# Kernel tuning notes

Hardware: AMD Instinct MI355X
Metric: run time of the kernel (lower is better)

The kernel has to match this reference:

```python
import jax, jax.numpy as jnp
import numpy as np
from jax import lax

B, T_Y, T_X = 16, 1600, 400
MEL_C, TXT_C, MAS_C = 80, 512, 384
HID = MAS_C * 2          # SwiGLUConvFFN hidden width (mas_channels*2)
NEG = -1e9


def setup_inputs() -> dict:
    key = jax.random.key(0)
    ks = jax.random.split(key, 20)
    p = lambda k, s: jax.random.normal(k, s, jnp.float32) * 0.02
    return {
        "mel_hidden_states": jax.random.normal(ks[0], (B, T_Y, MEL_C), jnp.float32),
        "text_hidden_states": jax.random.normal(ks[1], (B, T_X, TXT_C), jnp.float32),
        # mel SwiGLU conv-FFN (kernel 5): in->2*HID, gate, HID->MAS_C
        "mel_w1": p(ks[2], (2 * HID, MEL_C, 5)), "mel_b1": jnp.zeros((2 * HID,), jnp.float32),
        "mel_w2": p(ks[3], (MAS_C, HID, 5)),     "mel_b2": jnp.zeros((MAS_C,), jnp.float32),
        # text SwiGLU conv-FFN (kernel 3)
        "txt_w1": p(ks[4], (2 * HID, TXT_C, 3)), "txt_b1": jnp.zeros((2 * HID,), jnp.float32),
        "txt_w2": p(ks[5], (MAS_C, HID, 3)),     "txt_b2": jnp.zeros((MAS_C,), jnp.float32),
        # SimpleAttention query/key projections (value proj does not affect returned outputs)
        "wq": p(ks[6], (MAS_C, MAS_C)), "bq": jnp.zeros((MAS_C,), jnp.float32),
        "wk": p(ks[7], (MAS_C, MAS_C)), "bk": jnp.zeros((MAS_C,), jnp.float32),
        "x_lens": jax.random.randint(ks[8], (B,), T_X // 2, T_X + 1).astype(jnp.int32),
        "y_lens": jax.random.randint(ks[9], (B,), T_Y // 2, T_Y + 1).astype(jnp.int32),
    }


def _conv_ffn(x, pad_mask, w1, b1, w2, b2):
    """SwiGLU/ReGLU conv FFN. x:(B,T,C), pad_mask:(B,T) True=padded."""
    keep = (~pad_mask)[:, None, :].astype(x.dtype)          # (B,1,T)
    h = jnp.transpose(x, (0, 2, 1)) * keep                  # (B,C,T)
    dn = ("NCH", "OIH", "NCH")
    h = lax.conv_general_dilated(h, w1, (1,), "SAME", dimension_numbers=dn) + b1[None, :, None]
    a, g = jnp.split(h, 2, axis=1)
    h = a * jax.nn.relu(g) * keep                           # relugt gating
    h = lax.conv_general_dilated(h, w2, (1,), "SAME", dimension_numbers=dn) + b2[None, :, None]
    return jnp.transpose(h * keep, (0, 2, 1))               # (B,T,out)


def _mas_single(logp, t_x, t_y):
    """Glow-TTS maximum_path for one item. logp:(T_X,T_Y). Returns hard path (T_X,T_Y)."""
    xi = jnp.arange(T_X)
    yi = jnp.arange(T_Y)
    valid = (xi[:, None] < t_x) & (yi[None, :] < t_y) & (xi[:, None] <= yi[None, :])
    lp = jnp.where(valid, logp, NEG)

    def fstep(prev, col):                                   # prev:(T_X,), col:(T_X,)
        shifted = jnp.concatenate([jnp.full((1,), NEG, prev.dtype), prev[:-1]])
        cur = col + jnp.maximum(prev, shifted)
        return cur, cur

    init = jnp.where(xi == 0, 0.0, NEG).astype(logp.dtype)
    _, v = lax.scan(fstep, init, lp.T)                      # v:(T_Y,T_X) DP table

    def bstep(x, y):                                        # backtrack from y=T_Y-1 down
        active = y < t_y
        row = (xi == x) & active
        vp = v[y - 1]
        dec = (x > 0) & ((x == y) | (vp[jnp.maximum(x - 1, 0)] > vp[x]))
        new_x = jnp.where(active & (y > 0) & dec, x - 1, x)
        return new_x, row

    _, rows = lax.scan(bstep, t_x - 1, jnp.arange(T_Y - 1, -1, -1))
    return rows[::-1].T.astype(jnp.float32)                 # (T_X,T_Y)


def _safe_log(t, eps=1e-6):
    return jnp.nan_to_num(jnp.log(t + eps), nan=eps)


def reference(mel_hidden_states, text_hidden_states,
              mel_w1, mel_b1, mel_w2, mel_b2,
              txt_w1, txt_b1, txt_w2, txt_b2,
              wq, bq, wk, bk, x_lens, y_lens):
    x_mask = jnp.arange(T_X)[None, :] >= x_lens[:, None]    # (B,T_X) True=padded
    y_mask = jnp.arange(T_Y)[None, :] >= y_lens[:, None]    # (B,T_Y)

    text_proj = _conv_ffn(text_hidden_states, x_mask, txt_w1, txt_b1, txt_w2, txt_b2)
    mel_proj = _conv_ffn(mel_hidden_states, y_mask, mel_w1, mel_b1, mel_w2, mel_b2)

    q = mel_proj @ wq.T + bq                                # (B,T_Y,D)
    k = text_proj @ wk.T + bk                               # (B,T_X,D)
    scores = jnp.einsum("byd,bxd->byx", q, k) / (MAS_C ** 0.5)
    # expand_masks: mask==0 only where query AND key are both padded (faithful to source)
    both_pad = y_mask[:, :, None] & x_mask[:, None, :]
    scores = jnp.where(both_pad, jnp.float32(-1e-9), scores)
    attn_w = jax.nn.softmax(scores, axis=-1)                # (B,T_Y,T_X)

    avg_attn = attn_w[:, None]                              # (B,1,T_Y,T_X)
    attn_logprob = _safe_log(avg_attn)

    mas_in = jnp.transpose(attn_logprob[:, 0], (0, 2, 1))   # (B,T_X,T_Y)
    attn_hard = lax.stop_gradient(jax.vmap(_mas_single)(mas_in, x_lens, y_lens))
    attn_hard_dur = attn_hard.sum(2)                        # (B,T_X)
    return avg_attn, attn_logprob, attn_hard, attn_hard_dur
```

## Files before the change

### kernel.cpp

```cpp
#include <hip/hip_runtime.h>
#include <cstdint>

#define B 16
#define TY 1600
#define TX 400
#define MAS 384
#define HID 768
#define NEGV -1e9f

typedef __bf16 bf16x8 __attribute__((ext_vector_type(8)));
typedef float  f32x4  __attribute__((ext_vector_type(4)));
typedef float  f32x16 __attribute__((ext_vector_type(16)));

__device__ __forceinline__ f32x4 mfma16(bf16x8 a, bf16x8 b, f32x4 c) {
  return __builtin_amdgcn_mfma_f32_16x16x32_bf16(a, b, c, 0, 0, 0);
}
__device__ __forceinline__ f32x16 mfma32(bf16x8 a, bf16x8 b, f32x16 c) {
  return __builtin_amdgcn_mfma_f32_32x32x16_bf16(a, b, c, 0, 0, 0);
}

__global__ void split_pad_k(const float* __restrict__ in, __bf16* __restrict__ oh,
                            __bf16* __restrict__ ol, int CIN, int CINP, long n) {
  long i = (long)blockIdx.x * 256 + threadIdx.x;
  if (i >= n) return;
  long row = i / CINP; int ci = (int)(i - row * CINP);
  float v = (ci < CIN) ? in[row * CIN + ci] : 0.f;
  __bf16 h = (__bf16)v;
  oh[i] = h; ol[i] = (__bf16)(v - (float)h);
}

__global__ void wsplit_k(const float* __restrict__ w, __bf16* __restrict__ oh,
                         __bf16* __restrict__ ol, int CIN, int K_, int CINP, long n) {
  long i = (long)blockIdx.x * 256 + threadIdx.x;
  if (i >= n) return;
  long kdspan = (long)K_ * CINP;
  long nn = i / kdspan; int kd = (int)(i - nn * kdspan);
  int k = kd / CINP, ci = kd - k * CINP;
  float v = (ci < CIN) ? w[(nn * CIN + ci) * K_ + k] : 0.f;
  __bf16 h = (__bf16)v;
  oh[i] = h; ol[i] = (__bf16)(v - (float)h);
}

__global__ void tsplit_k(const float* __restrict__ in, __bf16* __restrict__ oh,
                         __bf16* __restrict__ ol, int JTOT, long n) {
  long i = (long)blockIdx.x * 256 + threadIdx.x;
  if (i >= n) return;
  int m = (int)(i / JTOT), j = (int)(i - (long)m * JTOT);
  float v = in[i];
  long o = (long)j * 384 + m;
  __bf16 h = (__bf16)v;
  oh[o] = h; ol[o] = (__bf16)(v - (float)h);
}

__global__ void fold_bias_k(const float* __restrict__ wq, const float* __restrict__ b,
                            float* __restrict__ o) {
  int n = threadIdx.x;
  float s = 0.f;
  for (int m = 0; m < 384; ++m) s = fmaf(wq[n * 384 + m], b[m], s);
  o[n] = s;
}

template<int KK>
__global__ __launch_bounds__(256)
void fold_mfma(const __bf16* __restrict__ xh, const __bf16* __restrict__ xl,
               const __bf16* __restrict__ wh, const __bf16* __restrict__ wl,
               __bf16* __restrict__ oh, __bf16* __restrict__ ol)
{
  constexpr int CINP = 384, ROWS = 64, STRIDE = 65;
  __shared__ float4 xs[8 * STRIDE];
  const int t0 = blockIdx.x * 64, n0 = blockIdx.y * 128;
  const int tid = threadIdx.x, wn = tid >> 6, lane = tid & 63;
  const int lr = lane & 15, lg = lane >> 4;
  const f32x4 Z4 = {0.f, 0.f, 0.f, 0.f};
  f32x4 acc[4][2];
  #pragma unroll
  for (int m = 0; m < 4; ++m) { acc[m][0] = Z4; acc[m][1] = Z4; }

  #pragma unroll 1
  for (int ci0 = 0; ci0 < CINP; ci0 += 32) {
    __syncthreads();
    for (int e = tid; e < ROWS * 8; e += 256) {
      int row = e >> 3, sc = e & 7, spl = sc >> 2, cg = sc & 3;
      int t = t0 + row;
      xs[(spl * 4 + cg) * STRIDE + row] =
          *(const float4*)((spl ? xl : xh) + (size_t)t * CINP + ci0 + cg * 8);
    }
    __syncthreads();
    bf16x8 ah[4], al[4];
    #pragma unroll
    for (int mf = 0; mf < 4; ++mf) {
      int row = mf * 16 + lr;
      ah[mf] = *(const bf16x8*)&xs[lg * STRIDE + row];
      al[mf] = *(const bf16x8*)&xs[(4 + lg) * STRIDE + row];
    }
    size_t kd = (size_t)ci0 + lg * 8;
    bf16x8 bh[2], bl[2];
    #pragma unroll
    for (int nf = 0; nf < 2; ++nf) {
      int nc = n0 + wn * 32 + nf * 16 + lr;
      bh[nf] = *(const bf16x8*)(wh + (size_t)nc * 384 + kd);
      bl[nf] = *(const bf16x8*)(wl + (size_t)nc * 384 + kd);
    }
    #pragma unroll
    for (int nf = 0; nf < 2; ++nf)
      #pragma unroll
      for (int mf = 0; mf < 4; ++mf) acc[mf][nf] = mfma16(ah[mf], bh[nf], acc[mf][nf]);
    #pragma unroll
    for (int nf = 0; nf < 2; ++nf)
      #pragma unroll
      for (int mf = 0; mf < 4; ++mf) acc[mf][nf] = mfma16(ah[mf], bl[nf], acc[mf][nf]);
    #pragma unroll
    for (int nf = 0; nf < 2; ++nf)
      #pragma unroll
      for (int mf = 0; mf < 4; ++mf) acc[mf][nf] = mfma16(al[mf], bh[nf], acc[mf][nf]);
  }
  #pragma unroll
  for (int nf = 0; nf < 2; ++nf) {
    int c = n0 + wn * 32 + nf * 16 + lr;
    #pragma unroll
    for (int mf = 0; mf < 4; ++mf) {
      #pragma unroll
      for (int r = 0; r < 4; ++r) {
        int j = t0 + mf * 16 + lg * 4 + r;
        int k = j % KK, ci = j / KK;
        size_t o = (size_t)((((ci >> 4) * KK + k) * 2 + ((ci >> 3) & 1)) * 3072)
                 + (size_t)c * 8 + (ci & 7);
        float v = acc[mf][nf][r];
        __bf16 vh = (__bf16)v;
        oh[o] = vh; ol[o] = (__bf16)(v - (float)vh);
      }
    }
  }
}

template<int CINP, int K, int T>
__global__ __launch_bounds__(256)
void conv1_mfma(const __bf16* __restrict__ xh, const __bf16* __restrict__ xl,
                const __bf16* __restrict__ wh, const __bf16* __restrict__ wl,
                const float* __restrict__ bias, const int* __restrict__ lens,
                __bf16* __restrict__ hh, __bf16* __restrict__ hl)
{
  constexpr int BM = 128, PAD = K / 2, ROWS = BM + K - 1, KD = K * CINP;
  __shared__ float4 xs[8 * ROWS];
  const int b = blockIdx.z, t0 = blockIdx.x * BM, n0 = blockIdx.y * 64;
  const int tid = threadIdx.x, wid = tid >> 6, lane = tid & 63;
  const int wm = wid >> 1, wn = wid & 1, lr = lane & 15, lg = lane >> 4;
  const int len = lens[b];
  const f32x4 Z4 = {0.f, 0.f, 0.f, 0.f};
  f32x4 acc_a[4][2], acc_g[4][2];
  #pragma unroll
  for (int m = 0; m < 4; ++m)
    #pragma unroll
    for (int n = 0; n < 2; ++n) { acc_a[m][n] = Z4; acc_g[m][n] = Z4; }

  #pragma unroll 1
  for (int ci0 = 0; ci0 < CINP; ci0 += 32) {
    __syncthreads();
    for (int e = tid; e < ROWS * 8; e += 256) {
      int row = e >> 3, sc = e & 7, spl = sc >> 2, cg = sc & 3;
      int t = t0 + row - PAD;
      float4 v = {0.f, 0.f, 0.f, 0.f};
      if (t >= 0 && t < len)
        v = *(const float4*)((spl ? xl : xh) + ((size_t)b * T + t) * CINP + ci0 + cg * 8);
      xs[(spl * 4 + cg) * ROWS + row] = v;
    }
    __syncthreads();
    #pragma unroll
    for (int k = 0; k < K; ++k) {
      bf16x8 ah[4], al[4];
      #pragma unroll
      for (int mf = 0; mf < 4; ++mf) {
        int row = wm * 64 + mf * 16 + lr + k;
        ah[mf] = *(const bf16x8*)&xs[lg * ROWS + row];
        al[mf] = *(const bf16x8*)&xs[(4 + lg) * ROWS + row];
      }
      size_t kd = (size_t)k * CINP + ci0 + lg * 8;
      #pragma unroll
      for (int nf = 0; nf < 2; ++nf) {
        int na = n0 + wn * 32 + nf * 16 + lr;
        bf16x8 bah = *(const bf16x8*)(wh + (size_t)na * KD + kd);
        bf16x8 bal = *(const bf16x8*)(wl + (size_t)na * KD + kd);
        bf16x8 bgh = *(const bf16x8*)(wh + (size_t)(na + HID) * KD + kd);
        bf16x8 bgl = *(const bf16x8*)(wl + (size_t)(na + HID) * KD + kd);
        #pragma unroll
        for (int mf = 0; mf < 4; ++mf) {
          acc_a[mf][nf] = mfma16(ah[mf], bah, acc_a[mf][nf]);
          acc_a[mf][nf] = mfma16(ah[mf], bal, acc_a[mf][nf]);
          acc_a[mf][nf] = mfma16(al[mf], bah, acc_a[mf][nf]);
          acc_g[mf][nf] = mfma16(ah[mf], bgh, acc_g[mf][nf]);
          acc_g[mf][nf] = mfma16(ah[mf], bgl, acc_g[mf][nf]);
          acc_g[mf][nf] = mfma16(al[mf], bgh, acc_g[mf][nf]);
        }
      }
    }
  }
  #pragma unroll
  for (int nf = 0; nf < 2; ++nf) {
    int c = n0 + wn * 32 + nf * 16 + lr;
    float ba = bias[c], bg = bias[c + HID];
    #pragma unroll
    for (int mf = 0; mf < 4; ++mf) {
      #pragma unroll
      for (int r = 0; r < 4; ++r) {
        int t = t0 + wm * 64 + mf * 16 + lg * 4 + r;
        if (t < T) {
          float a = acc_a[mf][nf][r] + ba;
          float g = acc_g[mf][nf][r] + bg;
          float v = a * fmaxf(g, 0.f);
          __bf16 vh = (__bf16)v;
          size_t o = ((size_t)b * T + t) * HID + c;
          hh[o] = vh;
          hl[o] = (__bf16)(v - (float)vh);
        }
      }
    }
  }
}

template<int K, int T, bool STORET>
__global__ __launch_bounds__(256)
void conv2_mfma(const __bf16* __restrict__ xh, const __bf16* __restrict__ xl,
                const __bf16* __restrict__ wh, const __bf16* __restrict__ wl,
                const float* __restrict__ bias, const float* __restrict__ ab,
                const int* __restrict__ lens, float* __restrict__ out)
{
  constexpr int CINP = 768, BM = 128, PAD = K / 2, ROWS = BM + K - 1, STRIDE = ROWS + 1;
  constexpr int BROWS = K * 2;
  __shared__ float4 xa[4 * STRIDE];
  __shared__ float4 bs[2 * BROWS * 192];
  const int b = blockIdx.z, t0 = blockIdx.x * BM, n0 = blockIdx.y * 192;
  const int tid = threadIdx.x, wid = tid >> 6, lane = tid & 63;
  const int wm = wid >> 1, wn = wid & 1, lc = lane & 31, lk = lane >> 5;
  const int len = lens[b];
  f32x16 acc[2][3];
  #pragma unroll
  for (int m = 0; m < 2; ++m)
    #pragma unroll
    for (int n = 0; n < 3; ++n)
      #pragma unroll
      for (int r = 0; r < 16; ++r) acc[m][n][r] = 0.f;

  #pragma unroll 1
  for (int s = 0; s < 48; ++s) {
    __syncthreads();
    for (int e = tid; e < ROWS * 4; e += 256) {
      int row = e >> 2, sc = e & 3, spl = sc >> 1, cg = sc & 1;
      int t = t0 + row - PAD;
      float4 v = {0.f, 0.f, 0.f, 0.f};
      if (t >= 0 && t < len)
        v = *(const float4*)((spl ? xl : xh) + ((size_t)b * T + t) * CINP + s * 16 + cg * 8);
      xa[(spl * 2 + cg) * STRIDE + row] = v;
    }
    for (int r = wid; r < 2 * BROWS; r += 4) {
      int spl = r / BROWS, rr = r - spl * BROWS;
      const char* src = (const char*)((spl ? wl : wh) + (size_t)(s * BROWS + rr) * 3072
                                      + (size_t)n0 * 8) + (size_t)lane * 16;
      char* dst = (char*)&bs[r * 192];
      #pragma unroll
      for (int i = 0; i < 3; ++i)
        __builtin_amdgcn_global_load_lds(
            (const __attribute__((address_space(1))) void*)(src + i * 1024),
            (__attribute__((address_space(3))) void*)(dst + i * 1024), 16, 0, 0);
    }
    __syncthreads();
    #pragma unroll
    for (int k = 0; k < K; ++k) {
      bf16x8 ah[2], al[2], bh[3], bl[3];
      #pragma unroll
      for (int mf = 0; mf < 2; ++mf) {
        int row = wm * 64 + mf * 32 + lc + k;
        ah[mf] = *(const bf16x8*)&xa[lk * STRIDE + row];
        al[mf] = *(const bf16x8*)&xa[(2 + lk) * STRIDE + row];
      }
      #pragma unroll
      for (int nf = 0; nf < 3; ++nf) {
        int col = wn * 96 + nf * 32 + lc;
        bh[nf] = *(const bf16x8*)&bs[(k * 2 + lk) * 192 + col];
        bl[nf] = *(const bf16x8*)&bs[(BROWS + k * 2 + lk) * 192 + col];
      }
      #pragma unroll
      for (int nf = 0; nf < 3; ++nf)
        #pragma unroll
        for (int mf = 0; mf < 2; ++mf)
          acc[mf][nf] = mfma32(ah[mf], bh[nf], acc[mf][nf]);
      #pragma unroll
      for (int nf = 0; nf < 3; ++nf)
        #pragma unroll
        for (int mf = 0; mf < 2; ++mf)
          acc[mf][nf] = mfma32(ah[mf], bl[nf], acc[mf][nf]);
      #pragma unroll
      for (int nf = 0; nf < 3; ++nf)
        #pragma unroll
        for (int mf = 0; mf < 2; ++mf)
          acc[mf][nf] = mfma32(al[mf], bh[nf], acc[mf][nf]);
    }
  }
  #pragma unroll
  for (int nf = 0; nf < 3; ++nf) {
    int c = n0 + wn * 96 + nf * 32 + lc;
    float bb = bias[c], aB = ab[c];
    #pragma unroll
    for (int mf = 0; mf < 2; ++mf) {
      #pragma unroll
      for (int r = 0; r < 16; ++r) {
        int t = t0 + wm * 64 + mf * 32 + (r & 3) + 8 * (r >> 2) + 4 * lk;
        if (t < T) {
          float v = acc[mf][nf][r] + bb;
          if (t >= len) v = 0.f;
          v += aB;
          if (STORET) out[((size_t)b * MAS + c) * T + t] = v;
          else        out[((size_t)b * T + t) * MAS + c] = v;
        }
      }
    }
  }
}

__global__ __launch_bounds__(512)
void scores_k(const float* __restrict__ q, const float* __restrict__ kT,
              const int* __restrict__ xl, const int* __restrict__ yl,
              float* __restrict__ oattn, float* __restrict__ ologp)
{
  __shared__ float qs[16 * 384];
  __shared__ float tmp[8];
  const int b = blockIdx.y, y0 = blockIdx.x * 16, tid = threadIdx.x;
  for (int e = tid; e < 16 * 384; e += 512)
    qs[e] = q[((size_t)b * TY + (y0 + e / 384)) * 384 + (e - (e / 384) * 384)];
  __syncthreads();
  float acc[16];
  #pragma unroll
  for (int i = 0; i < 16; ++i) acc[i] = 0.f;
  const int x = tid;
  if (x < TX) {
    const float* kb = kT + (size_t)b * MAS * TX + x;
    for (int d = 0; d < 384; d += 4) {
      float k0 = kb[(size_t)(d + 0) * TX], k1 = kb[(size_t)(d + 1) * TX];
      float k2 = kb[(size_t)(d + 2) * TX], k3 = kb[(size_t)(d + 3) * TX];
      #pragma unroll
      for (int yy = 0; yy < 16; ++yy) {
        float4 qv = *(const float4*)&qs[yy * 384 + d];
        acc[yy] = fmaf(qv.x, k0, fmaf(qv.y, k1, fmaf(qv.z, k2, fmaf(qv.w, k3, acc[yy]))));
      }
    }
  }
  const int xlen = xl[b], ylen = yl[b];
  const float scale = 0.05103103630798288f;
  const bool xpad = (x >= xlen);
  const int wv = tid >> 6, ln = tid & 63;
  #pragma unroll 1
  for (int yy = 0; yy < 16; ++yy) {
    int y = y0 + yy;
    float s = -3.0e38f;
    if (x < TX) {
      s = acc[yy] * scale;
      if (xpad && (y >= ylen)) s = -1e-9f;
    }
    float m = s;
    for (int off = 32; off; off >>= 1) m = fmaxf(m, __shfl_xor(m, off));
    if (ln == 0) tmp[wv] = m;
    __syncthreads();
    float mx = fmaxf(fmaxf(fmaxf(tmp[0], tmp[1]), fmaxf(tmp[2], tmp[3])),
                     fmaxf(fmaxf(tmp[4], tmp[5]), fmaxf(tmp[6], tmp[7])));
    __syncthreads();
    float e = (x < TX) ? expf(s - mx) : 0.f;
    float sm = e;
    for (int off = 32; off; off >>= 1) sm += __shfl_xor(sm, off);
    if (ln == 0) tmp[wv] = sm;
    __syncthreads();
    float tot = tmp[0] + tmp[1] + tmp[2] + tmp[3] + tmp[4] + tmp[5] + tmp[6] + tmp[7];
    __syncthreads();
    if (x < TX) {
      float w = e / tot;
      size_t o = ((size_t)b * TY + y) * TX + x;
      oattn[o] = w;
      ologp[o] = logf(w + 1e-6f);
    }
  }
}

#define MLD4(sbv, Lbuf) do {                                              \
    _Pragma("unroll")                                                     \
    for (int r_ = 0; r_ < 4; ++r_) {                                      \
      const int row_ = (sbv) * 4 + r_;                                    \
      Lbuf[r_][0] = *(const float2*)&half[row_ * 400 + a0];               \
      Lbuf[r_][1] = *(const float2*)&half[row_ * 400 + a1];               \
      Lbuf[r_][2] = *(const float2*)&half[row_ * 400 + a2];               \
    } } while (0)

#define MCMP4(sbv, Lbuf) do {                                             \
    _Pragma("unroll")                                                     \
    for (int r_ = 0; r_ < 4; ++r_) {                                      \
      const int y_ = ybase + (sbv) * 4 + r_;                              \
      float lp[6] = {Lbuf[r_][0].x + wxm[0], Lbuf[r_][0].y + wxm[1],      \
                     Lbuf[r_][1].x + wxm[2], Lbuf[r_][1].y + wxm[3],      \
                     Lbuf[r_][2].x + wxm[4], Lbuf[r_][2].y + wxm[5]};     \
      if (phase1) {                                                       \
        int c_ = y_ - p0;                                                 \
        _Pragma("unroll")                                                 \
        for (int j_ = 0; j_ < 6; ++j_) lp[j_] = (j_ <= c_) ? lp[j_] : NEGV; \
      }                                                                   \
      unsigned pr_ = ((w[3] > w[4]) ? 1u : 0u) | ((w[4] > w[5]) ? 2u : 0u); \
      p16 |= pr_ << ((y_ & 7) * 2);                                       \
      float nw[6];                                                        \
      nw[0] = lp[0] + w[0];                                               \
      _Pragma("unroll")                                                   \
      for (int j_ = 1; j_ < 6; ++j_) nw[j_] = lp[j_] + fmaxf(w[j_], w[j_ - 1]); \
      _Pragma("unroll")                                                   \
      for (int j_ = 0; j_ < 6; ++j_) w[j_] = nw[j_];                      \
    } } while (0)

#define FLUSHBITS(y7_) do {                                               \
    unsigned lo = 0, hi = 0;                                              \
    _Pragma("unroll")                                                     \
    for (int r2_ = 0; r2_ < 4; ++r2_) {                                   \
      lo |= ((p16 >> (2 * r2_)) & 3u) << (8 * r2_);                       \
      hi |= ((p16 >> (2 * r2_ + 8)) & 3u) << (8 * r2_);                   \
    }                                                                     \
    unsigned lo1 = (unsigned)__shfl_xor((int)lo, 1), hi1 = (unsigned)__shfl_xor((int)hi, 1); \
    lo |= lo1 << 2; hi |= hi1 << 2;                                       \
    unsigned lo2 = (unsigned)__shfl_xor((int)lo, 2), hi2 = (unsigned)__shfl_xor((int)hi, 2); \
    lo |= lo2 << 4; hi |= hi2 << 4;                                       \
    if ((GL & 3) == 0 && GL < 200) {                                      \
      unsigned long long E = (unsigned long long)lo | ((unsigned long long)hi << 32); \
      *(unsigned long long*)&lbits[(size_t)((y7_) >> 3) * 512 + (size_t)(GL >> 2) * 8] = E; \
    }                                                                     \
    p16 = 0; } while (0)

#define LBAR() do {                                                       \
    asm volatile("s_waitcnt lgkmcnt(0)" ::: "memory");                    \
    __builtin_amdgcn_sched_barrier(0);                                    \
    __builtin_amdgcn_s_barrier();                                         \
    __builtin_amdgcn_sched_barrier(0); } while (0)

#define PUBEX() do {                                                      \
    if (GL < 200) { vbuf[pb][2 * GL] = w[4]; vbuf[pb][2 * GL + 1] = w[5]; } \
    LBAR();                                                               \
    _Pragma("unroll")                                                     \
    for (int j_ = 0; j_ < 4; ++j_) {                                      \
      int x_ = p0 + j_;                                                   \
      w[j_] = (x_ >= 0 && GL < 200) ? vbuf[pb][x_] : NEGV;                \
    }                                                                     \
    pb ^= 1; } while (0)

__global__ __launch_bounds__(256, 1)
void mas_k(const float* __restrict__ logprob, const int* __restrict__ xl,
           const int* __restrict__ yl, float* __restrict__ hard, float* __restrict__ dur)
{
  __shared__ float ring[12800];
  __shared__ unsigned char lbits[102400];
  __shared__ float vbuf[2][400];
  const int b = blockIdx.x;
  const int tid = threadIdx.x, wid = tid >> 6;
  const int GL = tid;
  const int xlen = xl[b], ylen = yl[b];
  const float* lpb = logprob + (size_t)b * TY * TX;
  const int p0 = GL * 2 - 4;

  int a0 = p0, a1 = p0 + 2, a2 = p0 + 4;
  a0 = a0 < 0 ? 0 : (a0 > 398 ? 398 : a0);
  a1 = a1 < 0 ? 0 : (a1 > 398 ? 398 : a1);
  a2 = a2 < 0 ? 0 : (a2 > 398 ? 398 : a2);

  float w[6], wxm[6];
  #pragma unroll
  for (int j = 0; j < 6; ++j) {
    int x = p0 + j;
    wxm[j] = (x >= 0 && x < xlen) ? 0.f : NEGV;
    w[j] = (x == 0) ? 0.f : NEGV;
  }

  const char* lpc = (const char*)lpb;
  constexpr size_t maxgs = (size_t)TY * 1600 - 25600;
  char* ringc = (char*)ring;
  const int lane = tid & 63;
  auto issue_group = [&](int g) {
    size_t gs = (size_t)g * 25600; if (gs > maxgs) gs = maxgs;
    for (int c = wid; c < 25; c += 4)
      __builtin_amdgcn_global_load_lds(
          (const __attribute__((address_space(1))) void*)(lpc + gs + (size_t)c * 1024 + (size_t)lane * 16),
          (__attribute__((address_space(3))) void*)(ringc + (g & 1) * 25600 + c * 1024), 16, 0, 0);
  };

  issue_group(0);
  issue_group(1);

  int pb = 0;
  unsigned p16 = 0;
  const int ngroups = (ylen + 15) >> 4;
  #pragma unroll 1
  for (int g = 0; g < ngroups; ++g) {
    if (wid == 0) asm volatile("s_waitcnt vmcnt(7)" ::: "memory");
    else          asm volatile("s_waitcnt vmcnt(6)" ::: "memory");
    __builtin_amdgcn_sched_barrier(0);
    __builtin_amdgcn_s_barrier();
    __builtin_amdgcn_sched_barrier(0);
    const float* half = ring + (g & 1) * 6400;
    const int ybase = g * 16;
    const bool phase1 = (ybase < TX);
    float2 LA[4][3], LB[4][3];
    MLD4(0, LA);
    MCMP4(0, LA);
    MLD4(1, LB);
    PUBEX();
    MCMP4(1, LB);
    FLUSHBITS(ybase + 7);
    MLD4(2, LA);
    PUBEX();
    MCMP4(2, LA);
    MLD4(3, LB);
    PUBEX();
    MCMP4(3, LB);
    FLUSHBITS(ybase + 15);
    PUBEX();
    __builtin_amdgcn_sched_barrier(0);
    issue_group(g + 2);
  }

  __syncthreads();
  if (wid != 0) return;

  int x = xlen - 1;
  int cnt = 0;
  float* hb = hard + (size_t)b * TX * TY;
  float* db = dur + (size_t)b * TX;

  #pragma unroll 1
  for (int ycur = ylen - 1; ycur >= 0; ycur -= 64) {
    int lo = x - 63; if (lo < 0) lo = 0;
    const int wb = (lo >> 3) & ~3;
    int ry = ycur - lane;
    unsigned w0 = 0, w1 = 0, w2 = 0;
    if (ry >= 0) {
      const unsigned char* p = lbits + (size_t)(ry >> 3) * 512 + (ry & 7);
      unsigned bt_[12];
      #pragma unroll
      for (int j = 0; j < 12; ++j) bt_[j] = p[(size_t)(wb + j) * 8];
      w0 = bt_[0] | (bt_[1] << 8) | (bt_[2] << 16) | (bt_[3] << 24);
      w1 = bt_[4] | (bt_[5] << 8) | (bt_[6] << 16) | (bt_[7] << 24);
      w2 = bt_[8] | (bt_[9] << 8) | (bt_[10] << 16) | (bt_[11] << 24);
    }
    const int rows = (ycur + 1 < 64) ? (ycur + 1) : 64;
    #pragma unroll 1
    for (int s = 0; s < rows; s += 8) {
      const int cnt8 = (rows - s < 8) ? (rows - s) : 8;
      unsigned r0[8], r1[8], r2[8];
      #pragma unroll
      for (int u = 0; u < 8; ++u) {
        r0[u] = (unsigned)__builtin_amdgcn_readlane((int)w0, s + u);
        r1[u] = (unsigned)__builtin_amdgcn_readlane((int)w1, s + u);
        r2[u] = (unsigned)__builtin_amdgcn_readlane((int)w2, s + u);
      }
      #pragma unroll
      for (int u = 0; u < 8; ++u) {
        if (u < cnt8) {
          const int yy = ycur - s - u;
          ++cnt;
          if (yy > 0 && x > 0) {
            const int boff = (x >> 3) - wb;
            const unsigned word = (boff < 4) ? r0[u] : ((boff < 8) ? r1[u] : r2[u]);
            const unsigned byte = word >> ((boff & 3) * 8);
            if ((x == yy) || ((byte >> (x & 7)) & 1)) {
              for (int q = lane; q < cnt; q += 64) hb[(size_t)x * TY + yy + q] = 1.0f;
              if (lane == 0) db[x] = (float)cnt;
              cnt = 0;
              --x;
            }
          }
        }
      }
    }
  }
  for (int q = lane; q < cnt; q += 64) hb[(size_t)x * TY + q] = 1.0f;
  if (lane == 0) db[x] = (float)cnt;
}

extern "C" void kernel_launch(void* const* d_in, const int* in_sizes, int n_in,
                              void* d_out, int out_size, void* d_ws, size_t ws_size,
                              hipStream_t stream) {
  const float* mel_x  = (const float*)d_in[0];
  const float* txt_x  = (const float*)d_in[1];
  const float* mel_w1 = (const float*)d_in[2];
  const float* mel_b1 = (const float*)d_in[3];
  const float* mel_w2 = (const float*)d_in[4];
  const float* mel_b2 = (const float*)d_in[5];
  const float* txt_w1 = (const float*)d_in[6];
  const float* txt_b1 = (const float*)d_in[7];
  const float* txt_w2 = (const float*)d_in[8];
  const float* txt_b2 = (const float*)d_in[9];
  const float* wq     = (const float*)d_in[10];
  const float* bq     = (const float*)d_in[11];
  const float* wk     = (const float*)d_in[12];
  const float* bk     = (const float*)d_in[13];
  const int*   xl     = (const int*)d_in[14];
  const int*   yl     = (const int*)d_in[15];

  char* wsb = (char*)d_ws;
  constexpr size_t MXH   = 0;
  constexpr size_t MXL   = MXH   + 4915200;
  constexpr size_t TXH   = MXL   + 4915200;
  constexpr size_t TXL   = TXH   + 6553600;
  constexpr size_t KTF   = TXH;
  constexpr size_t WFMH  = TXL   + 6553600;
  constexpr size_t WFML  = WFMH  + 2949120;
  constexpr size_t WFTH  = WFML  + 2949120;
  constexpr size_t WFTL  = WFTH  + 1769472;
  constexpr size_t B2M   = WFTL  + 1769472;
  constexpr size_t B2T   = B2M   + 2048;
  constexpr size_t HH    = B2T   + 2048;
  constexpr size_t HL    = HH    + 39321600;
  constexpr size_t SCR   = HL    + 39321600;
  constexpr size_t W1MH  = SCR;
  constexpr size_t W1ML  = W1MH  + 1474560;
  constexpr size_t W1TH  = W1ML  + 1474560;
  constexpr size_t W1TL  = W1TH  + 4718592;
  constexpr size_t WQH   = W1TL  + 4718592;
  constexpr size_t WQL   = WQH   + 294912;
  constexpr size_t WKH   = WQL   + 294912;
  constexpr size_t WKL   = WKH   + 294912;
  constexpr size_t W2TMH = WKL   + 294912;
  constexpr size_t W2TML = W2TMH + 2949120;
  constexpr size_t W2TTH = W2TML + 2949120;
  constexpr size_t W2TTL = W2TTH + 1769472;
  constexpr size_t QF    = SCR;

  float* out = (float*)d_out;
  float* o_attn = out;
  float* o_logp = out + (size_t)10240000;
  float* o_hard = out + (size_t)20480000;
  float* o_dur  = out + (size_t)30720000;

  hipMemsetAsync(o_hard, 0, (size_t)(10240000 + 6400) * sizeof(float), stream);

  split_pad_k<<<9600, 256, 0, stream>>>(mel_x, (__bf16*)(wsb + MXH), (__bf16*)(wsb + MXL), 80, 96, 2457600L);
  split_pad_k<<<12800, 256, 0, stream>>>(txt_x, (__bf16*)(wsb + TXH), (__bf16*)(wsb + TXL), 512, 512, 3276800L);
  wsplit_k<<<2880, 256, 0, stream>>>(mel_w1, (__bf16*)(wsb + W1MH), (__bf16*)(wsb + W1ML), 80, 5, 96, 737280L);
  wsplit_k<<<9216, 256, 0, stream>>>(txt_w1, (__bf16*)(wsb + W1TH), (__bf16*)(wsb + W1TL), 512, 3, 512, 2359296L);
  wsplit_k<<<576, 256, 0, stream>>>(wq, (__bf16*)(wsb + WQH), (__bf16*)(wsb + WQL), 384, 1, 384, 147456L);
  wsplit_k<<<576, 256, 0, stream>>>(wk, (__bf16*)(wsb + WKH), (__bf16*)(wsb + WKL), 384, 1, 384, 147456L);
  tsplit_k<<<5760, 256, 0, stream>>>(mel_w2, (__bf16*)(wsb + W2TMH), (__bf16*)(wsb + W2TML), 3840, 1474560L);
  tsplit_k<<<3456, 256, 0, stream>>>(txt_w2, (__bf16*)(wsb + W2TTH), (__bf16*)(wsb + W2TTL), 2304, 884736L);
  fold_mfma<5><<<dim3(60, 3), 256, 0, stream>>>(
      (const __bf16*)(wsb + W2TMH), (const __bf16*)(wsb + W2TML),
      (const __bf16*)(wsb + WQH), (const __bf16*)(wsb + WQL),
      (__bf16*)(wsb + WFMH), (__bf16*)(wsb + WFML));
  fold_mfma<3><<<dim3(36, 3), 256, 0, stream>>>(
      (const __bf16*)(wsb + W2TTH), (const __bf16*)(wsb + W2TTL),
      (const __bf16*)(wsb + WKH), (const __bf16*)(wsb + WKL),
      (__bf16*)(wsb + WFTH), (__bf16*)(wsb + WFTL));
  fold_bias_k<<<1, 384, 0, stream>>>(wq, mel_b2, (float*)(wsb + B2M));
  fold_bias_k<<<1, 384, 0, stream>>>(wk, txt_b2, (float*)(wsb + B2T));

  conv1_mfma<512, 3, 400><<<dim3(4, 12, B), 256, 0, stream>>>(
      (const __bf16*)(wsb + TXH), (const __bf16*)(wsb + TXL),
      (const __bf16*)(wsb + W1TH), (const __bf16*)(wsb + W1TL),
      txt_b1, xl, (__bf16*)(wsb + HH), (__bf16*)(wsb + HL));
  conv2_mfma<3, 400, true><<<dim3(4, 2, B), 256, 0, stream>>>(
      (const __bf16*)(wsb + HH), (const __bf16*)(wsb + HL),
      (const __bf16*)(wsb + WFTH), (const __bf16*)(wsb + WFTL),
      (const float*)(wsb + B2T), bk, xl, (float*)(wsb + KTF));

  conv1_mfma<96, 5, 1600><<<dim3(13, 12, B), 256, 0, stream>>>(
      (const __bf16*)(wsb + MXH), (const __bf16*)(wsb + MXL),
      (const __bf16*)(wsb + W1MH), (const __bf16*)(wsb + W1ML),
      mel_b1, yl, (__bf16*)(wsb + HH), (__bf16*)(wsb + HL));
  conv2_mfma<5, 1600, false><<<dim3(13, 2, B), 256, 0, stream>>>(
      (const __bf16*)(wsb + HH), (const __bf16*)(wsb + HL),
      (const __bf16*)(wsb + WFMH), (const __bf16*)(wsb + WFML),
      (const float*)(wsb + B2M), bq, yl, (float*)(wsb + QF));

  scores_k<<<dim3(100, B), 512, 0, stream>>>(
      (const float*)(wsb + QF), (const float*)(wsb + KTF), xl, yl, o_attn, o_logp);
  mas_k<<<B, 256, 0, stream>>>(o_logp, xl, yl, o_hard, o_dur);
}
```

Baseline: 1.435 ms.

## Widen MAS halo to cut barrier exchanges and split backtrack kernel

```diff
diff --git a/kernel.cpp b/kernel.cpp
--- a/kernel.cpp
+++ b/kernel.cpp
@@ -378,35 +378,44 @@
   }
 }
 
-#define MLD4(sbv, Lbuf) do {                                              \
+#define LBAR() do {                                                       \
+    asm volatile("s_waitcnt lgkmcnt(0)" ::: "memory");                    \
+    __builtin_amdgcn_sched_barrier(0);                                    \
+    __builtin_amdgcn_s_barrier();                                         \
+    __builtin_amdgcn_sched_barrier(0); } while (0)
+
+#define MLD8(h0_, Lb) do {                                                \
     _Pragma("unroll")                                                     \
-    for (int r_ = 0; r_ < 4; ++r_) {                                      \
-      const int row_ = (sbv) * 4 + r_;                                    \
-      Lbuf[r_][0] = *(const float2*)&half[row_ * 400 + a0];               \
-      Lbuf[r_][1] = *(const float2*)&half[row_ * 400 + a1];               \
-      Lbuf[r_][2] = *(const float2*)&half[row_ * 400 + a2];               \
+    for (int r_ = 0; r_ < 8; ++r_) {                                      \
+      const int row_ = (h0_) + r_;                                        \
+      _Pragma("unroll")                                                   \
+      for (int i_ = 0; i_ < 5; ++i_)                                      \
+        Lb[r_][i_] = *(const float2*)&half[row_ * 400 + a[i_]];           \
     } } while (0)
 
-#define MCMP4(sbv, Lbuf) do {                                             \
+#define MCMP8(h0_, Lb) do {                                               \
     _Pragma("unroll")                                                     \
-    for (int r_ = 0; r_ < 4; ++r_) {                                      \
-      const int y_ = ybase + (sbv) * 4 + r_;                              \
-      float lp[6] = {Lbuf[r_][0].x + wxm[0], Lbuf[r_][0].y + wxm[1],      \
-                     Lbuf[r_][1].x + wxm[2], Lbuf[r_][1].y + wxm[3],      \
-                     Lbuf[r_][2].x + wxm[4], Lbuf[r_][2].y + wxm[5]};     \
+    for (int r_ = 0; r_ < 8; ++r_) {                                      \
+      const int y_ = ybase + (h0_) + r_;                                  \
+      float lp[10];                                                       \
+      _Pragma("unroll")                                                   \
+      for (int i_ = 0; i_ < 5; ++i_) {                                    \
+        lp[2 * i_]     = Lb[r_][i_].x + wxm[2 * i_];                      \
+        lp[2 * i_ + 1] = Lb[r_][i_].y + wxm[2 * i_ + 1];                  \
+      }                                                                   \
       if (phase1) {                                                       \
         int c_ = y_ - p0;                                                 \
         _Pragma("unroll")                                                 \
-        for (int j_ = 0; j_ < 6; ++j_) lp[j_] = (j_ <= c_) ? lp[j_] : NEGV; \
+        for (int j_ = 0; j_ < 10; ++j_) lp[j_] = (j_ <= c_) ? lp[j_] : NEGV; \
       }                                                                   \
-      unsigned pr_ = ((w[3] > w[4]) ? 1u : 0u) | ((w[4] > w[5]) ? 2u : 0u); \
+      unsigned pr_ = ((w[7] > w[8]) ? 1u : 0u) | ((w[8] > w[9]) ? 2u : 0u); \
       p16 |= pr_ << ((y_ & 7) * 2);                                       \
-      float nw[6];                                                        \
+      float nw[10];                                                       \
       nw[0] = lp[0] + w[0];                                               \
       _Pragma("unroll")                                                   \
-      for (int j_ = 1; j_ < 6; ++j_) nw[j_] = lp[j_] + fmaxf(w[j_], w[j_ - 1]); \
+      for (int j_ = 1; j_ < 10; ++j_) nw[j_] = lp[j_] + fmaxf(w[j_], w[j_ - 1]); \
       _Pragma("unroll")                                                   \
-      for (int j_ = 0; j_ < 6; ++j_) w[j_] = nw[j_];                      \
+      for (int j_ = 0; j_ < 10; ++j_) w[j_] = nw[j_];                     \
     } } while (0)
 
 #define FLUSHBITS(y7_) do {                                               \
@@ -422,48 +431,44 @@
     lo |= lo2 << 4; hi |= hi2 << 4;                                       \
     if ((GL & 3) == 0 && GL < 200) {                                      \
       unsigned long long E = (unsigned long long)lo | ((unsigned long long)hi << 32); \
-      *(unsigned long long*)&lbits[(size_t)((y7_) >> 3) * 512 + (size_t)(GL >> 2) * 8] = E; \
+      *(unsigned long long*)&bb8[(size_t)((y7_) >> 3) * 512 + (size_t)(GL >> 2) * 8] = E; \
     }                                                                     \
     p16 = 0; } while (0)
 
-#define LBAR() do {                                                       \
-    asm volatile("s_waitcnt lgkmcnt(0)" ::: "memory");                    \
-    __builtin_amdgcn_sched_barrier(0);                                    \
-    __builtin_amdgcn_s_barrier();                                         \
-    __builtin_amdgcn_sched_barrier(0); } while (0)
-
 #define PUBEX() do {                                                      \
-    if (GL < 200) { vbuf[pb][2 * GL] = w[4]; vbuf[pb][2 * GL + 1] = w[5]; } \
+    if (GL < 200) { vbuf[pb][2 * GL] = w[8]; vbuf[pb][2 * GL + 1] = w[9]; } \
     LBAR();                                                               \
     _Pragma("unroll")                                                     \
-    for (int j_ = 0; j_ < 4; ++j_) {                                      \
+    for (int j_ = 0; j_ < 8; ++j_) {                                      \
       int x_ = p0 + j_;                                                   \
       w[j_] = (x_ >= 0 && GL < 200) ? vbuf[pb][x_] : NEGV;                \
     }                                                                     \
     pb ^= 1; } while (0)
 
 __global__ __launch_bounds__(256, 1)
-void mas_k(const float* __restrict__ logprob, const int* __restrict__ xl,
-           const int* __restrict__ yl, float* __restrict__ hard, float* __restrict__ dur)
+void mas_fwd(const float* __restrict__ logprob, const int* __restrict__ xl,
+             const int* __restrict__ yl, unsigned char* __restrict__ bits)
 {
   __shared__ float ring[12800];
-  __shared__ unsigned char lbits[102400];
   __shared__ float vbuf[2][400];
   const int b = blockIdx.x;
-  const int tid = threadIdx.x, wid = tid >> 6;
+  const int tid = threadIdx.x, wid = tid >> 6, lane = tid & 63;
   const int GL = tid;
   const int xlen = xl[b], ylen = yl[b];
   const float* lpb = logprob + (size_t)b * TY * TX;
-  const int p0 = GL * 2 - 4;
-
-  int a0 = p0, a1 = p0 + 2, a2 = p0 + 4;
-  a0 = a0 < 0 ? 0 : (a0 > 398 ? 398 : a0);
-  a1 = a1 < 0 ? 0 : (a1 > 398 ? 398 : a1);
-  a2 = a2 < 0 ? 0 : (a2 > 398 ? 398 : a2);
-
-  float w[6], wxm[6];
-  #pragma unroll
-  for (int j = 0; j < 6; ++j) {
+  unsigned char* bb8 = bits + (size_t)b * 102400;
+  const int p0 = GL * 2 - 8;
+
+  int a[5];
+  #pragma unroll
+  for (int i = 0; i < 5; ++i) {
+    int t = p0 + 2 * i;
+    a[i] = t < 0 ? 0 : (t > 398 ? 398 : t);
+  }
+
+  float w[10], wxm[10];
+  #pragma unroll
+  for (int j = 0; j < 10; ++j) {
     int x = p0 + j;
     wxm[j] = (x >= 0 && x < xlen) ? 0.f : NEGV;
     w[j] = (x == 0) ? 0.f : NEGV;
@@ -472,7 +477,6 @@
   const char* lpc = (const char*)lpb;
   constexpr size_t maxgs = (size_t)TY * 1600 - 25600;
   char* ringc = (char*)ring;
-  const int lane = tid & 63;
   auto issue_group = [&](int g) {
     size_t gs = (size_t)g * 25600; if (gs > maxgs) gs = maxgs;
     for (int c = wid; c < 25; c += 4)
@@ -497,33 +501,33 @@
     const float* half = ring + (g & 1) * 6400;
     const int ybase = g * 16;
     const bool phase1 = (ybase < TX);
-    float2 LA[4][3], LB[4][3];
-    MLD4(0, LA);
-    MCMP4(0, LA);
-    MLD4(1, LB);
+    float2 L[8][5];
+    MLD8(0, L);
+    MCMP8(0, L);
+    FLUSHBITS(ybase + 7);
     PUBEX();
-    MCMP4(1, LB);
-    FLUSHBITS(ybase + 7);
-    MLD4(2, LA);
-    PUBEX();
-    MCMP4(2, LA);
-    MLD4(3, LB);
-    PUBEX();
-    MCMP4(3, LB);
+    MLD8(8, L);
+    MCMP8(8, L);
     FLUSHBITS(ybase + 15);
     PUBEX();
     __builtin_amdgcn_sched_barrier(0);
     issue_group(g + 2);
   }
-
-  __syncthreads();
-  if (wid != 0) return;
+}
+
+__global__ __launch_bounds__(64)
+void mas_bt(const unsigned char* __restrict__ bits, const int* __restrict__ xl,
+            const int* __restrict__ yl, float* __restrict__ hard, float* __restrict__ dur)
+{
+  const int b = blockIdx.x;
+  const int lane = threadIdx.x;
+  const int xlen = xl[b], ylen = yl[b];
+  const unsigned char* bb8 = bits + (size_t)b * 102400;
+  float* hb = hard + (size_t)b * TX * TY;
+  float* db = dur + (size_t)b * TX;
 
   int x = xlen - 1;
   int cnt = 0;
-  float* hb = hard + (size_t)b * TX * TY;
-  float* db = dur + (size_t)b * TX;
-
   #pragma unroll 1
   for (int ycur = ylen - 1; ycur >= 0; ycur -= 64) {
     int lo = x - 63; if (lo < 0) lo = 0;
@@ -531,7 +535,7 @@
     int ry = ycur - lane;
     unsigned w0 = 0, w1 = 0, w2 = 0;
     if (ry >= 0) {
-      const unsigned char* p = lbits + (size_t)(ry >> 3) * 512 + (ry & 7);
+      const unsigned char* p = bb8 + (size_t)(ry >> 3) * 512 + (ry & 7);
       unsigned bt_[12];
       #pragma unroll
       for (int j = 0; j < 12; ++j) bt_[j] = p[(size_t)(wb + j) * 8];
@@ -608,6 +612,7 @@
   constexpr size_t B2T   = B2M   + 2048;
   constexpr size_t HH    = B2T   + 2048;
   constexpr size_t HL    = HH    + 39321600;
+  constexpr size_t BITS  = MXH;
   constexpr size_t SCR   = HL    + 39321600;
   constexpr size_t W1MH  = SCR;
   constexpr size_t W1ML  = W1MH  + 1474560;
@@ -670,5 +675,6 @@
 
   scores_k<<<dim3(100, B), 512, 0, stream>>>(
       (const float*)(wsb + QF), (const float*)(wsb + KTF), xl, yl, o_attn, o_logp);
-  mas_k<<<B, 256, 0, stream>>>(o_logp, xl, yl, o_hard, o_dur);
-}
+  mas_fwd<<<B, 256, 0, stream>>>(o_logp, xl, yl, (unsigned char*)(wsb + BITS));
+  mas_bt<<<B, 64, 0, stream>>>((const unsigned char*)(wsb + BITS), xl, yl, o_hard, o_dur);
+}
```

Result: slower. 1.472 ms (+2.6%).
